# Kernel optimization log

Measured on AMD Instinct MI355X. Metric: run time of the kernel, lower is better.

## Reference

```python
import jax, jax.numpy as jnp
import numpy as np

B, C, O, K, H, W, CH = 32, 256, 256, 3, 56, 56, 4  # batch, in_planes, out_planes, kernel, spatial, in_chunk
STRIDE, PAD, DIL = 1, 1, 1


def setup_inputs() -> dict:
    key = jax.random.key(0)
    ks = jax.random.split(key, 5)
    gain = np.sqrt(2.0).astype(np.float32)  # calculate_gain('relu')
    x = jax.random.normal(ks[0], (B, C, H, W), jnp.float32)
    # CWFF: fc1 1x1 conv (C->C, no bias), fc2 1x1 conv (C->CH*C, bias)
    fc1_w = jax.random.normal(ks[1], (C, C), jnp.float32) * np.sqrt(2.0 / C).astype(np.float32)  # kaiming fan_out
    fc2_w = jax.random.normal(ks[2], (CH * C, C), jnp.float32) * np.sqrt(2.0 / (CH * C)).astype(np.float32)
    fc2_b = jnp.zeros((CH * C,), jnp.float32)
    cog_weight = jax.random.normal(ks[3], (O, CH, K, K), jnp.float32) * (gain * (CH * K * K) ** -0.5)
    weight = jax.random.normal(ks[4], (O, C, K, K), jnp.float32) * (gain * (C * K * K) ** -0.5)
    return dict(x=x, fc1_w=fc1_w, fc2_w=fc2_w, fc2_b=fc2_b, cog_weight=cog_weight, weight=weight)


def reference(x, fc1_w, fc2_w, fc2_b, cog_weight, weight):
    # CWFF: global avg pool -> 1x1 conv -> relu -> 1x1 conv
    pooled = x.mean(axis=(2, 3))                       # [B, C]
    h = jax.nn.relu(pooled @ fc1_w.T)                  # [B, C]
    kern = h @ fc2_w.T + fc2_b                         # [B, CH*C]
    # torch view(-1, in_chunk, 1, 1): channel dim splits as (c, ch)
    kern = kern.reshape(B, C, CH)                      # [B, C, CH]
    # cognitive weights: conv2d(cog_weight, kernel) == contraction over in_chunk
    cw = jnp.einsum('bct,otij->bocij', kern, cog_weight)   # [B, O, C, K, K]
    dyn_w = jax.nn.sigmoid(cw) * weight[None]               # per-sample kernels [B, O, C, K, K]
    # per-sample conv (groups=B in the original grouped-conv trick)
    def conv1(xi, wi):
        return jax.lax.conv_general_dilated(
            xi[None], wi,
            window_strides=(STRIDE, STRIDE),
            padding=[(PAD, PAD), (PAD, PAD)],
            rhs_dilation=(DIL, DIL))[0]
    return jax.vmap(conv1)(x, dyn_w)                   # [B, O, H, W]
```

## Files before the change

kernel.cpp:

```cpp
#include <hip/hip_runtime.h>

typedef unsigned short u16;
typedef __attribute__((ext_vector_type(4))) float f32x4;
typedef __attribute__((ext_vector_type(8))) short s16x8;
typedef __attribute__((ext_vector_type(4))) unsigned short u16x4;

static __device__ __forceinline__ u16 f2bf(float f) {
    unsigned int x = __float_as_uint(f);
    x += 0x7fffu + ((x >> 16) & 1u);
    return (u16)(x >> 16);
}

__global__ __launch_bounds__(256) void pool_kernel(const float* __restrict__ x,
                                                   float* __restrict__ pooled) {
    int bc = blockIdx.x;
    const float* p = x + (size_t)bc * 3136;
    float s = 0.f;
    for (int i = threadIdx.x; i < 784; i += 256) {
        f32x4 v = *(const f32x4*)(p + i * 4);
        s += v.x + v.y + v.z + v.w;
    }
#pragma unroll
    for (int off = 32; off; off >>= 1) s += __shfl_xor(s, off);
    __shared__ float red[4];
    int lane = threadIdx.x & 63, wave = threadIdx.x >> 6;
    if (lane == 0) red[wave] = s;
    __syncthreads();
    if (threadIdx.x == 0)
        pooled[bc] = (red[0] + red[1] + red[2] + red[3]) * (1.0f / 3136.0f);
}

__global__ __launch_bounds__(256) void fc1_kernel(const float* __restrict__ pooled,
                                                  const float* __restrict__ w,
                                                  float* __restrict__ h) {
    __shared__ float pv[256];
    int b = blockIdx.x >> 6;
    pv[threadIdx.x] = pooled[b * 256 + threadIdx.x];
    __syncthreads();
    int lane = threadIdx.x & 63, wave = threadIdx.x >> 6;
    int i = ((blockIdx.x & 63) << 2) + wave;
    f32x4 v = *(const f32x4*)(w + i * 256 + lane * 4);
    float s = v.x * pv[lane * 4 + 0] + v.y * pv[lane * 4 + 1] +
              v.z * pv[lane * 4 + 2] + v.w * pv[lane * 4 + 3];
#pragma unroll
    for (int off = 32; off; off >>= 1) s += __shfl_xor(s, off);
    if (lane == 0) h[b * 256 + i] = fmaxf(s, 0.f);
}

__global__ __launch_bounds__(256) void fc2_kernel(const float* __restrict__ h,
                                                  const float* __restrict__ w,
                                                  const float* __restrict__ bias,
                                                  float* __restrict__ kern) {
    __shared__ float hv[256];
    int b = blockIdx.x >> 8;
    hv[threadIdx.x] = h[b * 256 + threadIdx.x];
    __syncthreads();
    int lane = threadIdx.x & 63, wave = threadIdx.x >> 6;
    int i = ((blockIdx.x & 255) << 2) + wave;
    f32x4 v = *(const f32x4*)(w + i * 256 + lane * 4);
    float s = v.x * hv[lane * 4 + 0] + v.y * hv[lane * 4 + 1] +
              v.z * hv[lane * 4 + 2] + v.w * hv[lane * 4 + 3];
#pragma unroll
    for (int off = 32; off; off >>= 1) s += __shfl_xor(s, off);
    if (lane == 0) kern[b * 1024 + i] = s + bias[i];
}

__global__ __launch_bounds__(256) void dynw_kernel(const float* __restrict__ kern,
                                                   const float* __restrict__ cogw,
                                                   const float* __restrict__ wgt,
                                                   u16* __restrict__ dynw) {
    __shared__ float wl[2304];
    const int o = blockIdx.x & 255;
    const int bg = blockIdx.x >> 8;
    const int c = threadIdx.x;
    const float* wo = wgt + (size_t)o * 2304;
#pragma unroll
    for (int j = 0; j < 9; ++j)
        wl[j * 256 + c] = wo[j * 256 + c];
    __syncthreads();

    float cg0[9], cg1[9], cg2[9], cg3[9];
#pragma unroll
    for (int p = 0; p < 9; ++p) {
        cg0[p] = cogw[(o * 4 + 0) * 9 + p];
        cg1[p] = cogw[(o * 4 + 1) * 9 + p];
        cg2[p] = cogw[(o * 4 + 2) * 9 + p];
        cg3[p] = cogw[(o * 4 + 3) * 9 + p];
    }
    float w9[9];
#pragma unroll
    for (int p = 0; p < 9; ++p) w9[p] = wl[c * 9 + p];

    for (int b = bg * 8; b < bg * 8 + 8; ++b) {
        f32x4 k4 = *(const f32x4*)(kern + b * 1024 + c * 4);
        u16* dst = dynw + (size_t)(b * 256 + o) * 9 * 256 + c;
#pragma unroll
        for (int p = 0; p < 9; ++p) {
            float cw = k4.x * cg0[p] + k4.y * cg1[p] + k4.z * cg2[p] + k4.w * cg3[p];
            float sg = 1.0f / (1.0f + __expf(-cw));
            dst[p * 256] = f2bf(sg * w9[p]);
        }
    }
}

#define LDSW 40
__global__ __launch_bounds__(256, 3) void conv_kernel(const float* __restrict__ x,
                                                      const u16* __restrict__ dynw,
                                                      float* __restrict__ out) {
    __shared__ u16 lds[4 * 58 * LDSW];
    const int tid = threadIdx.x;
    const int wave = tid >> 6, lane = tid & 63;
    const int l15 = lane & 15, quad = lane >> 4;
    const int gid = blockIdx.x;
    const int slot = gid >> 3;
    const int b = (gid & 7) * 4 + slot / 56;
    const int s2 = slot % 56;
    const int stile = s2 >> 1;
    const int oh = s2 & 1;
    const int y0 = stile * 2;

    if (tid < 64) {
        int side = tid & 1, yy = (tid >> 1) & 3, cg = tid >> 3;
        *(u16x4*)&lds[(yy * 58 + (side ? 57 : 0)) * LDSW + cg * 4] = (u16x4){0, 0, 0, 0};
    }

    f32x4 acc[2][7];
#pragma unroll
    for (int mf = 0; mf < 2; ++mf)
#pragma unroll
        for (int nf = 0; nf < 7; ++nf) acc[mf][nf] = (f32x4){0.f, 0.f, 0.f, 0.f};

    int bbase[7];
#pragma unroll
    for (int nf = 0; nf < 7; ++nf) {
        int n = nf * 16 + l15;
        int r = (n >= 56) ? 1 : 0;
        int xx = n - 56 * r;
        bbase[nf] = (r * 58 + xx) * LDSW + quad * 8;
    }
    const u16* Abase = dynw + ((size_t)b * 256 + oh * 128 + wave * 32 + l15) * 2304 + quad * 8;
    const float* Xb = x + (size_t)b * 256 * 3136;

    __syncthreads();
    for (int cc = 0; cc < 8; ++cc) {
#pragma unroll
        for (int it = 0; it < 7; ++it) {
            int i = it * 256 + tid;
            int q = i / 56;
            int xx = i - q * 56;
            int yy = q & 3;
            int cg = q >> 2;
            int yg = y0 - 1 + yy;
            u16x4 w = (u16x4){0, 0, 0, 0};
            if ((unsigned)yg < 56u) {
                const float* src = Xb + (size_t)(cc * 32 + cg * 4) * 3136 + yg * 56 + xx;
                w.x = f2bf(src[0]);
                w.y = f2bf(src[3136]);
                w.z = f2bf(src[2 * 3136]);
                w.w = f2bf(src[3 * 3136]);
            }
            *(u16x4*)&lds[(yy * 58 + 1 + xx) * LDSW + cg * 4] = w;
        }
        __syncthreads();
#pragma unroll
        for (int p = 0; p < 9; ++p) {
            const int dy = p / 3, dx = p % 3;
            const int tapoff = (dy * 58 + dx) * LDSW;
            s16x8 a0 = *(const s16x8*)(Abase + 0 * 36864 + p * 256 + cc * 32);
            s16x8 a1 = *(const s16x8*)(Abase + 1 * 36864 + p * 256 + cc * 32);
#pragma unroll
            for (int nf = 0; nf < 7; ++nf) {
                s16x8 bf = *(const s16x8*)(&lds[bbase[nf] + tapoff]);
                acc[0][nf] = __builtin_amdgcn_mfma_f32_16x16x32_bf16(a0, bf, acc[0][nf], 0, 0, 0);
                acc[1][nf] = __builtin_amdgcn_mfma_f32_16x16x32_bf16(a1, bf, acc[1][nf], 0, 0, 0);
            }
        }
        __syncthreads();
    }
#pragma unroll
    for (int mf = 0; mf < 2; ++mf) {
        int o = oh * 128 + wave * 32 + mf * 16 + quad * 4;
        size_t obase = ((size_t)b * 256 + o) * 3136 + (size_t)stile * 112 + l15;
#pragma unroll
        for (int nf = 0; nf < 7; ++nf) {
#pragma unroll
            for (int r = 0; r < 4; ++r)
                out[obase + (size_t)r * 3136 + nf * 16] = acc[mf][nf][r];
        }
    }
}

extern "C" void kernel_launch(void* const* d_in, const int* in_sizes, int n_in,
                              void* d_out, int out_size, void* d_ws, size_t ws_size,
                              hipStream_t stream) {
    const float* x    = (const float*)d_in[0];
    const float* fc1w = (const float*)d_in[1];
    const float* fc2w = (const float*)d_in[2];
    const float* fc2b = (const float*)d_in[3];
    const float* cogw = (const float*)d_in[4];
    const float* wgt  = (const float*)d_in[5];
    float* out = (float*)d_out;

    char* ws = (char*)d_ws;
    float* pooled = (float*)ws;
    float* h      = (float*)(ws + 32768);
    float* kern   = (float*)(ws + 65536);
    u16*   dynw   = (u16*)(ws + 196608);

    pool_kernel<<<8192, 256, 0, stream>>>(x, pooled);
    fc1_kernel<<<2048, 256, 0, stream>>>(pooled, fc1w, h);
    fc2_kernel<<<8192, 256, 0, stream>>>(h, fc2w, fc2b, kern);
    dynw_kernel<<<1024, 256, 0, stream>>>(kern, cogw, wgt, dynw);
    conv_kernel<<<1792, 256, 0, stream>>>(x, dynw, out);
}
```

Baseline: 368.1 us.

## Reuse LDS B-fragments across horizontal taps and stage epilogue through LDS

Each lane now owns 7 consecutive output pixels (n = l15*7+nf) instead of strided ones. For each kernel row it loads 9 contiguous B fragments once and reuses them across the three horizontal taps, which cuts LDS reads from 63 to 27 per channel chunk. The output mapping changes, so the epilogue writes accumulators to an LDS buffer and then stores coalesced rows to global memory. The trade-off is more registers for the 9 held fragments, a larger shared buffer (about 29 KB) that may limit occupancy, and extra barriers in the epilogue.

```diff
diff --git a/kernel.cpp b/kernel.cpp
--- a/kernel.cpp
+++ b/kernel.cpp
@@ -107,7 +107,8 @@
 __global__ __launch_bounds__(256, 3) void conv_kernel(const float* __restrict__ x,
                                                       const u16* __restrict__ dynw,
                                                       float* __restrict__ out) {
-    __shared__ u16 lds[4 * 58 * LDSW];
+    __shared__ __align__(16) char smem[28928];
+    u16* lds16 = (u16*)smem;
     const int tid = threadIdx.x;
     const int wave = tid >> 6, lane = tid & 63;
     const int l15 = lane & 15, quad = lane >> 4;
@@ -121,7 +122,7 @@
 
     if (tid < 64) {
         int side = tid & 1, yy = (tid >> 1) & 3, cg = tid >> 3;
-        *(u16x4*)&lds[(yy * 58 + (side ? 57 : 0)) * LDSW + cg * 4] = (u16x4){0, 0, 0, 0};
+        *(u16x4*)&lds16[(yy * 58 + (side ? 57 : 0)) * LDSW + cg * 4] = (u16x4){0, 0, 0, 0};
     }
 
     f32x4 acc[2][7];
@@ -130,14 +131,11 @@
 #pragma unroll
         for (int nf = 0; nf < 7; ++nf) acc[mf][nf] = (f32x4){0.f, 0.f, 0.f, 0.f};
 
-    int bbase[7];
-#pragma unroll
-    for (int nf = 0; nf < 7; ++nf) {
-        int n = nf * 16 + l15;
-        int r = (n >= 56) ? 1 : 0;
-        int xx = n - 56 * r;
-        bbase[nf] = (r * 58 + xx) * LDSW + quad * 8;
-    }
+    const int n0 = l15 * 7;
+    const int r0 = (n0 >= 56) ? 1 : 0;
+    const int xx0 = n0 - 56 * r0;
+    const int hbase = (r0 * 58 + xx0) * LDSW + quad * 8;
+
     const u16* Abase = dynw + ((size_t)b * 256 + oh * 128 + wave * 32 + l15) * 2304 + quad * 8;
     const float* Xb = x + (size_t)b * 256 * 3136;
 
@@ -159,33 +157,51 @@
                 w.z = f2bf(src[2 * 3136]);
                 w.w = f2bf(src[3 * 3136]);
             }
-            *(u16x4*)&lds[(yy * 58 + 1 + xx) * LDSW + cg * 4] = w;
-        }
-        __syncthreads();
-#pragma unroll
-        for (int p = 0; p < 9; ++p) {
-            const int dy = p / 3, dx = p % 3;
-            const int tapoff = (dy * 58 + dx) * LDSW;
-            s16x8 a0 = *(const s16x8*)(Abase + 0 * 36864 + p * 256 + cc * 32);
-            s16x8 a1 = *(const s16x8*)(Abase + 1 * 36864 + p * 256 + cc * 32);
-#pragma unroll
-            for (int nf = 0; nf < 7; ++nf) {
-                s16x8 bf = *(const s16x8*)(&lds[bbase[nf] + tapoff]);
-                acc[0][nf] = __builtin_amdgcn_mfma_f32_16x16x32_bf16(a0, bf, acc[0][nf], 0, 0, 0);
-                acc[1][nf] = __builtin_amdgcn_mfma_f32_16x16x32_bf16(a1, bf, acc[1][nf], 0, 0, 0);
+            *(u16x4*)&lds16[(yy * 58 + 1 + xx) * LDSW + cg * 4] = w;
+        }
+        __syncthreads();
+#pragma unroll
+        for (int dy = 0; dy < 3; ++dy) {
+            s16x8 H[9];
+#pragma unroll
+            for (int t = 0; t < 9; ++t)
+                H[t] = *(const s16x8*)(&lds16[hbase + (dy * 58 + t) * LDSW]);
+#pragma unroll
+            for (int dx = 0; dx < 3; ++dx) {
+                const int p = dy * 3 + dx;
+                s16x8 a0 = *(const s16x8*)(Abase + 0 * 36864 + p * 256 + cc * 32);
+                s16x8 a1 = *(const s16x8*)(Abase + 1 * 36864 + p * 256 + cc * 32);
+#pragma unroll
+                for (int nf = 0; nf < 7; ++nf) {
+                    acc[0][nf] = __builtin_amdgcn_mfma_f32_16x16x32_bf16(a0, H[nf + dx], acc[0][nf], 0, 0, 0);
+                    acc[1][nf] = __builtin_amdgcn_mfma_f32_16x16x32_bf16(a1, H[nf + dx], acc[1][nf], 0, 0, 0);
+                }
             }
         }
         __syncthreads();
     }
+
+    float* ep = (float*)smem;
 #pragma unroll
     for (int mf = 0; mf < 2; ++mf) {
-        int o = oh * 128 + wave * 32 + mf * 16 + quad * 4;
-        size_t obase = ((size_t)b * 256 + o) * 3136 + (size_t)stile * 112 + l15;
+        __syncthreads();
 #pragma unroll
         for (int nf = 0; nf < 7; ++nf) {
-#pragma unroll
-            for (int r = 0; r < 4; ++r)
-                out[obase + (size_t)r * 3136 + nf * 16] = acc[mf][nf][r];
+            int s = l15 * 7 + nf;
+#pragma unroll
+            for (int r = 0; r < 4; ++r) {
+                int ol = wave * 16 + quad * 4 + r;
+                ep[ol * 113 + s] = acc[mf][nf][r];
+            }
+        }
+        __syncthreads();
+#pragma unroll
+        for (int j = 0; j < 28; ++j) {
+            int idx = j * 256 + tid;
+            int ol = idx / 112;
+            int s = idx - ol * 112;
+            int o = oh * 128 + (ol >> 4) * 32 + mf * 16 + (ol & 15);
+            out[((size_t)b * 256 + o) * 3136 + (size_t)y0 * 56 + s] = ep[ol * 113 + s];
         }
     }
 }
```

After: 396.6 us. 7.7% more time.

## Pre-transpose input to padded NHWC bf16 and read conv B operand from global

Applied to the files above, without the earlier changes.

Adds a transpose kernel that converts x to a zero-padded channels-last bf16 buffer. The conv kernel then loads MFMA B fragments straight from global memory instead of staging them through LDS, which drops the per-chunk conversion, the LDS writes and the barriers. Occupancy is raised to 4 blocks per CU. The cost is an extra kernel pass and global/L2 traffic in place of LDS reuse across the nine taps.

```diff
diff --git a/kernel.cpp b/kernel.cpp
--- a/kernel.cpp
+++ b/kernel.cpp
@@ -4,6 +4,7 @@
 typedef __attribute__((ext_vector_type(4))) float f32x4;
 typedef __attribute__((ext_vector_type(8))) short s16x8;
 typedef __attribute__((ext_vector_type(4))) unsigned short u16x4;
+typedef __attribute__((ext_vector_type(8))) unsigned short u16x8;
 
 static __device__ __forceinline__ u16 f2bf(float f) {
     unsigned int x = __float_as_uint(f);
@@ -103,11 +104,47 @@
     }
 }
 
-#define LDSW 40
-__global__ __launch_bounds__(256, 3) void conv_kernel(const float* __restrict__ x,
+__global__ __launch_bounds__(256) void xpose_kernel(const float* __restrict__ x,
+                                                    u16* __restrict__ xT) {
+    const int gid = blockIdx.x;
+    const int cg = gid & 3;
+    const int yp = (gid >> 2) % 58;
+    const int b = gid / (4 * 58);
+    u16* dst = xT + ((size_t)b * 58 + yp) * 58 * 256 + cg * 64;
+    const int t = threadIdx.x;
+
+    if (yp == 0 || yp == 57) {
+        for (int i = t; i < 464; i += 256) {
+            int xcol = i >> 3, k = i & 7;
+            *(u16x8*)(dst + (size_t)xcol * 256 + k * 8) = (u16x8)(0);
+        }
+        return;
+    }
+    __shared__ float tile[64][57];
+    const float* src = x + ((size_t)(b * 256 + cg * 64) * 56 + (yp - 1)) * 56;
+    for (int i = t; i < 64 * 56; i += 256) {
+        int cr = i / 56, xcol = i - cr * 56;
+        tile[cr][xcol] = src[(size_t)cr * 3136 + xcol];
+    }
+    if (t < 16) {
+        int side = t >> 3, k = t & 7;
+        *(u16x8*)(dst + (size_t)(side ? 57 : 0) * 256 + k * 8) = (u16x8)(0);
+    }
+    __syncthreads();
+    for (int i = t; i < 896; i += 256) {
+        int xcol = i >> 4, c4 = i & 15;
+        u16x4 v;
+        v.x = f2bf(tile[c4 * 4 + 0][xcol]);
+        v.y = f2bf(tile[c4 * 4 + 1][xcol]);
+        v.z = f2bf(tile[c4 * 4 + 2][xcol]);
+        v.w = f2bf(tile[c4 * 4 + 3][xcol]);
+        *(u16x4*)(dst + (size_t)(xcol + 1) * 256 + c4 * 4) = v;
+    }
+}
+
+__global__ __launch_bounds__(256, 4) void conv_kernel(const u16* __restrict__ xT,
                                                       const u16* __restrict__ dynw,
                                                       float* __restrict__ out) {
-    __shared__ u16 lds[4 * 58 * LDSW];
     const int tid = threadIdx.x;
     const int wave = tid >> 6, lane = tid & 63;
     const int l15 = lane & 15, quad = lane >> 4;
@@ -119,63 +156,41 @@
     const int oh = s2 & 1;
     const int y0 = stile * 2;
 
-    if (tid < 64) {
-        int side = tid & 1, yy = (tid >> 1) & 3, cg = tid >> 3;
-        *(u16x4*)&lds[(yy * 58 + (side ? 57 : 0)) * LDSW + cg * 4] = (u16x4){0, 0, 0, 0};
-    }
-
     f32x4 acc[2][7];
 #pragma unroll
     for (int mf = 0; mf < 2; ++mf)
 #pragma unroll
         for (int nf = 0; nf < 7; ++nf) acc[mf][nf] = (f32x4){0.f, 0.f, 0.f, 0.f};
 
-    int bbase[7];
+    int rowcol[7];
 #pragma unroll
     for (int nf = 0; nf < 7; ++nf) {
         int n = nf * 16 + l15;
         int r = (n >= 56) ? 1 : 0;
         int xx = n - 56 * r;
-        bbase[nf] = (r * 58 + xx) * LDSW + quad * 8;
-    }
+        rowcol[nf] = (y0 + r) * 58 + xx;
+    }
+    const u16* Bbase = xT + (size_t)b * 58 * 58 * 256 + quad * 8;
     const u16* Abase = dynw + ((size_t)b * 256 + oh * 128 + wave * 32 + l15) * 2304 + quad * 8;
-    const float* Xb = x + (size_t)b * 256 * 3136;
-
-    __syncthreads();
+
+#pragma unroll 1
     for (int cc = 0; cc < 8; ++cc) {
 #pragma unroll
-        for (int it = 0; it < 7; ++it) {
-            int i = it * 256 + tid;
-            int q = i / 56;
-            int xx = i - q * 56;
-            int yy = q & 3;
-            int cg = q >> 2;
-            int yg = y0 - 1 + yy;
-            u16x4 w = (u16x4){0, 0, 0, 0};
-            if ((unsigned)yg < 56u) {
-                const float* src = Xb + (size_t)(cc * 32 + cg * 4) * 3136 + yg * 56 + xx;
-                w.x = f2bf(src[0]);
-                w.y = f2bf(src[3136]);
-                w.z = f2bf(src[2 * 3136]);
-                w.w = f2bf(src[3 * 3136]);
+        for (int dy = 0; dy < 3; ++dy) {
+#pragma unroll
+            for (int dx = 0; dx < 3; ++dx) {
+                const int p = dy * 3 + dx;
+                s16x8 a0 = *(const s16x8*)(Abase + 0 * 36864 + p * 256 + cc * 32);
+                s16x8 a1 = *(const s16x8*)(Abase + 1 * 36864 + p * 256 + cc * 32);
+#pragma unroll
+                for (int nf = 0; nf < 7; ++nf) {
+                    const u16* bp = Bbase + ((size_t)(rowcol[nf] + dy * 58 + dx) << 8) + cc * 32;
+                    s16x8 bf = *(const s16x8*)bp;
+                    acc[0][nf] = __builtin_amdgcn_mfma_f32_16x16x32_bf16(a0, bf, acc[0][nf], 0, 0, 0);
+                    acc[1][nf] = __builtin_amdgcn_mfma_f32_16x16x32_bf16(a1, bf, acc[1][nf], 0, 0, 0);
+                }
             }
-            *(u16x4*)&lds[(yy * 58 + 1 + xx) * LDSW + cg * 4] = w;
-        }
-        __syncthreads();
-#pragma unroll
-        for (int p = 0; p < 9; ++p) {
-            const int dy = p / 3, dx = p % 3;
-            const int tapoff = (dy * 58 + dx) * LDSW;
-            s16x8 a0 = *(const s16x8*)(Abase + 0 * 36864 + p * 256 + cc * 32);
-            s16x8 a1 = *(const s16x8*)(Abase + 1 * 36864 + p * 256 + cc * 32);
-#pragma unroll
-            for (int nf = 0; nf < 7; ++nf) {
-                s16x8 bf = *(const s16x8*)(&lds[bbase[nf] + tapoff]);
-                acc[0][nf] = __builtin_amdgcn_mfma_f32_16x16x32_bf16(a0, bf, acc[0][nf], 0, 0, 0);
-                acc[1][nf] = __builtin_amdgcn_mfma_f32_16x16x32_bf16(a1, bf, acc[1][nf], 0, 0, 0);
-            }
-        }
-        __syncthreads();
+        }
     }
 #pragma unroll
     for (int mf = 0; mf < 2; ++mf) {
@@ -206,10 +221,12 @@
     float* h      = (float*)(ws + 32768);
     float* kern   = (float*)(ws + 65536);
     u16*   dynw   = (u16*)(ws + 196608);
-
+    u16*   xT     = (u16*)(ws + 37945344);
+
+    xpose_kernel<<<7424, 256, 0, stream>>>(x, xT);
     pool_kernel<<<8192, 256, 0, stream>>>(x, pooled);
     fc1_kernel<<<2048, 256, 0, stream>>>(pooled, fc1w, h);
     fc2_kernel<<<8192, 256, 0, stream>>>(h, fc2w, fc2b, kern);
     dynw_kernel<<<1024, 256, 0, stream>>>(kern, cogw, wgt, dynw);
-    conv_kernel<<<1792, 256, 0, stream>>>(x, dynw, out);
-}
+    conv_kernel<<<1792, 256, 0, stream>>>(xT, dynw, out);
+}
```

Measured after the change: 1.075 ms. 192% more time.
